# Kernel tuning notes

Measured on AMD Instinct MI355X. Metric: run time of the kernel, lower is better.

Reference implementation:

```python
import jax, jax.numpy as jnp
import numpy as np

N = 2_000_000  # number of Gaussians


def setup_inputs() -> dict:
    key = jax.random.key(0)
    k1, k2, k3 = jax.random.split(key, 3)
    quaternions = jax.random.normal(k1, (N, 4), dtype=jnp.float32)
    scales = jax.random.normal(k2, (N, 3), dtype=jnp.float32) * 0.5
    opacities = jax.random.normal(k3, (N, 1), dtype=jnp.float32)
    return {"quaternions": quaternions, "scales": scales, "opacities": opacities}


def quaternion_to_rotation_matrix(q):
    # q: [N,4] with layout (w, x, y, z) as in the torch source
    w, x, y, z = q[:, 0], q[:, 1], q[:, 2], q[:, 3]
    xx, yy, zz = x * x, y * y, z * z
    xy, xz, yz = x * y, x * z, y * z
    xw, yw, zw = x * w, y * w, z * w
    r0 = jnp.stack([1 - 2 * (yy + zz), 2 * (xy - zw), 2 * (xz + yw)], axis=-1)
    r1 = jnp.stack([2 * (xy + zw), 1 - 2 * (xx + zz), 2 * (yz - xw)], axis=-1)
    r2 = jnp.stack([2 * (xz - yw), 2 * (yz + xw), 1 - 2 * (xx + yy)], axis=-1)
    return jnp.stack([r0, r1, r2], axis=-2)  # [N,3,3]


def reference(quaternions, scales, opacities):
    # sigmoid applied to raw opacities (source: 1/(1+exp(-o)))
    opac = jax.nn.sigmoid(opacities)
    # NOTE: source normalizes by the GLOBAL Frobenius norm of the whole tensor
    # (to.linalg.norm with no dim) -- replicated faithfully.
    qn = quaternions / jnp.linalg.norm(quaternions)
    R = quaternion_to_rotation_matrix(qn)  # [N,3,3]
    # scales_d = (diag(exp(s)))**2 ; scales_i_d = (diag(1/exp(s)))**2
    s2 = jnp.exp(2.0 * scales)      # [N,3] diagonal of S^2
    inv_s2 = jnp.exp(-2.0 * scales)  # [N,3] diagonal of S^-2
    # cov = R @ diag(s2) @ R^T, inv_cov = R @ diag(inv_s2) @ R^T (closed form,
    # no batched 3x3 matmul chain / LAPACK inverse needed)
    cov = jnp.einsum('nij,nj,nkj->nik', R, s2, R)
    inv_cov = jnp.einsum('nij,nj,nkj->nik', R, inv_s2, R)
    return cov, inv_cov, opac
```

## Files before the change

kernel.cpp:

```cpp
#include <hip/hip_runtime.h>
#include <math.h>

#define RBLOCKS 1024
#define RTHREADS 256

__global__ __launch_bounds__(RTHREADS) void gp_reduce_sq(
    const float4* __restrict__ q4, int n4, double* __restrict__ partials) {
    __shared__ double sdata[RTHREADS];
    double acc = 0.0;
    int stride = gridDim.x * blockDim.x;
    for (int i = blockIdx.x * blockDim.x + threadIdx.x; i < n4; i += stride) {
        float4 v = q4[i];
        acc += (double)v.x * v.x + (double)v.y * v.y +
               (double)v.z * v.z + (double)v.w * v.w;
    }
    sdata[threadIdx.x] = acc;
    __syncthreads();
    for (int s = RTHREADS / 2; s > 0; s >>= 1) {
        if (threadIdx.x < s) sdata[threadIdx.x] += sdata[threadIdx.x + s];
        __syncthreads();
    }
    if (threadIdx.x == 0) partials[blockIdx.x] = sdata[0];
}

__global__ __launch_bounds__(RTHREADS) void gp_finalize_norm(
    const double* __restrict__ partials, float* __restrict__ inv_norm) {
    __shared__ double sdata[RTHREADS];
    double acc = 0.0;
    for (int i = threadIdx.x; i < RBLOCKS; i += RTHREADS) acc += partials[i];
    sdata[threadIdx.x] = acc;
    __syncthreads();
    for (int s = RTHREADS / 2; s > 0; s >>= 1) {
        if (threadIdx.x < s) sdata[threadIdx.x] += sdata[threadIdx.x + s];
        __syncthreads();
    }
    if (threadIdx.x == 0) *inv_norm = (float)(1.0 / sqrt(sdata[0]));
}

__global__ __launch_bounds__(256) void gp_main(
    const float4* __restrict__ q,
    const float* __restrict__ scales,
    const float* __restrict__ opac_in,
    const float* __restrict__ inv_norm_p,
    float* __restrict__ cov,
    float* __restrict__ inv_cov,
    float* __restrict__ opac_out,
    int n) {
    const float inv_norm = *inv_norm_p;
    int stride = gridDim.x * blockDim.x;
    for (int i = blockIdx.x * blockDim.x + threadIdx.x; i < n; i += stride) {
        float4 qi = q[i];
        float w = qi.x * inv_norm;
        float x = qi.y * inv_norm;
        float y = qi.z * inv_norm;
        float z = qi.w * inv_norm;

        float xx = x * x, yy = y * y, zz = z * z;
        float xy = x * y, xz = x * z, yz = y * z;
        float xw = x * w, yw = y * w, zw = z * w;

        float r00 = 1.f - 2.f * (yy + zz);
        float r01 = 2.f * (xy - zw);
        float r02 = 2.f * (xz + yw);
        float r10 = 2.f * (xy + zw);
        float r11 = 1.f - 2.f * (xx + zz);
        float r12 = 2.f * (yz - xw);
        float r20 = 2.f * (xz - yw);
        float r21 = 2.f * (yz + xw);
        float r22 = 1.f - 2.f * (xx + yy);

        float s0 = scales[3 * (size_t)i];
        float s1 = scales[3 * (size_t)i + 1];
        float s2 = scales[3 * (size_t)i + 2];

        float e0 = expf(2.f * s0), e1 = expf(2.f * s1), e2 = expf(2.f * s2);
        float f0 = expf(-2.f * s0), f1 = expf(-2.f * s1), f2 = expf(-2.f * s2);

        size_t base = (size_t)i * 9;

        {
            float a0 = r00 * e0, a1 = r01 * e1, a2 = r02 * e2;
            float b0 = r10 * e0, b1 = r11 * e1, b2 = r12 * e2;
            float c0 = r20 * e0, c1 = r21 * e1, c2 = r22 * e2;
            float m00 = a0 * r00 + a1 * r01 + a2 * r02;
            float m01 = a0 * r10 + a1 * r11 + a2 * r12;
            float m02 = a0 * r20 + a1 * r21 + a2 * r22;
            float m11 = b0 * r10 + b1 * r11 + b2 * r12;
            float m12 = b0 * r20 + b1 * r21 + b2 * r22;
            float m22 = c0 * r20 + c1 * r21 + c2 * r22;
            cov[base + 0] = m00;
            cov[base + 1] = m01;
            cov[base + 2] = m02;
            cov[base + 3] = m01;
            cov[base + 4] = m11;
            cov[base + 5] = m12;
            cov[base + 6] = m02;
            cov[base + 7] = m12;
            cov[base + 8] = m22;
        }
        {
            float a0 = r00 * f0, a1 = r01 * f1, a2 = r02 * f2;
            float b0 = r10 * f0, b1 = r11 * f1, b2 = r12 * f2;
            float c0 = r20 * f0, c1 = r21 * f1, c2 = r22 * f2;
            float m00 = a0 * r00 + a1 * r01 + a2 * r02;
            float m01 = a0 * r10 + a1 * r11 + a2 * r12;
            float m02 = a0 * r20 + a1 * r21 + a2 * r22;
            float m11 = b0 * r10 + b1 * r11 + b2 * r12;
            float m12 = b0 * r20 + b1 * r21 + b2 * r22;
            float m22 = c0 * r20 + c1 * r21 + c2 * r22;
            inv_cov[base + 0] = m00;
            inv_cov[base + 1] = m01;
            inv_cov[base + 2] = m02;
            inv_cov[base + 3] = m01;
            inv_cov[base + 4] = m11;
            inv_cov[base + 5] = m12;
            inv_cov[base + 6] = m02;
            inv_cov[base + 7] = m12;
            inv_cov[base + 8] = m22;
        }
        {
            float o = opac_in[i];
            opac_out[i] = 1.f / (1.f + expf(-o));
        }
    }
}

extern "C" void kernel_launch(void* const* d_in, const int* in_sizes, int n_in,
                              void* d_out, int out_size, void* d_ws, size_t ws_size,
                              hipStream_t stream) {
    const float* q = (const float*)d_in[0];
    const float* scales = (const float*)d_in[1];
    const float* opac = (const float*)d_in[2];
    int n = in_sizes[0] / 4;
    int n4 = in_sizes[0] / 4;

    float* out = (float*)d_out;
    float* cov = out;
    float* inv_cov = out + (size_t)n * 9;
    float* opac_out = out + (size_t)n * 18;

    double* partials = (double*)d_ws;
    float* inv_norm = (float*)((char*)d_ws + RBLOCKS * sizeof(double));

    gp_reduce_sq<<<RBLOCKS, RTHREADS, 0, stream>>>(
        (const float4*)q, n4, partials);
    gp_finalize_norm<<<1, RTHREADS, 0, stream>>>(partials, inv_norm);

    int blocks = 2048;
    gp_main<<<blocks, 256, 0, stream>>>(
        (const float4*)q, scales, opac, inv_norm,
        cov, inv_cov, opac_out, n);
}
```

Before: 51.31 us.

## Stage outputs through LDS for coalesced stores and fold norm finalize into main

The main kernel now processes one 256-element chunk per block. Scales are loaded as float4 into shared memory, and both 3x3 outputs are staged in LDS and written back as coalesced float4 stores, replacing stride-9 scalar stores. The separate finalize-norm launch is removed: every block re-reduces the 1024 double partials itself to get the inverse norm. The inverse exponentials are computed as reciprocals of the forward exps. In exchange, the kernel uses more LDS and has redundant per-block reduction work, and the grid grows to about 7800 blocks.

```diff
diff --git a/kernel.cpp b/kernel.cpp
--- a/kernel.cpp
+++ b/kernel.cpp
@@ -3,6 +3,7 @@
 
 #define RBLOCKS 1024
 #define RTHREADS 256
+#define CHUNK 256
 
 __global__ __launch_bounds__(RTHREADS) void gp_reduce_sq(
     const float4* __restrict__ q4, int n4, double* __restrict__ partials) {
@@ -23,33 +24,61 @@
     if (threadIdx.x == 0) partials[blockIdx.x] = sdata[0];
 }
 
-__global__ __launch_bounds__(RTHREADS) void gp_finalize_norm(
-    const double* __restrict__ partials, float* __restrict__ inv_norm) {
-    __shared__ double sdata[RTHREADS];
-    double acc = 0.0;
-    for (int i = threadIdx.x; i < RBLOCKS; i += RTHREADS) acc += partials[i];
-    sdata[threadIdx.x] = acc;
-    __syncthreads();
-    for (int s = RTHREADS / 2; s > 0; s >>= 1) {
-        if (threadIdx.x < s) sdata[threadIdx.x] += sdata[threadIdx.x + s];
-        __syncthreads();
-    }
-    if (threadIdx.x == 0) *inv_norm = (float)(1.0 / sqrt(sdata[0]));
-}
-
 __global__ __launch_bounds__(256) void gp_main(
     const float4* __restrict__ q,
     const float* __restrict__ scales,
     const float* __restrict__ opac_in,
-    const float* __restrict__ inv_norm_p,
+    const double* __restrict__ partials,
     float* __restrict__ cov,
     float* __restrict__ inv_cov,
     float* __restrict__ opac_out,
     int n) {
-    const float inv_norm = *inv_norm_p;
-    int stride = gridDim.x * blockDim.x;
-    for (int i = blockIdx.x * blockDim.x + threadIdx.x; i < n; i += stride) {
-        float4 qi = q[i];
+    __shared__ union SU {
+        double red[4];
+        float mat[2 * CHUNK * 9];
+    } u;
+    __shared__ float s_sc[CHUNK * 3];
+
+    const int tid = threadIdx.x;
+    const int c0 = blockIdx.x * CHUNK;
+    const int count = min(CHUNK, n - c0);
+
+    float4 qi = make_float4(0.f, 0.f, 0.f, 0.f);
+    float op = 0.f;
+    if (tid < count) {
+        qi = q[c0 + tid];
+        op = opac_in[c0 + tid];
+    }
+    const int nsf = count * 3;
+    const int nsf4 = nsf >> 2;
+    const float4* sc4 = (const float4*)(scales + (size_t)c0 * 3);
+    float4 sv = make_float4(0.f, 0.f, 0.f, 0.f);
+    if (tid < nsf4) sv = sc4[tid];
+
+    double acc = 0.0;
+#pragma unroll
+    for (int k = 0; k < RBLOCKS / 256; ++k) acc += partials[tid + 256 * k];
+#pragma unroll
+    for (int off = 32; off > 0; off >>= 1) acc += __shfl_down(acc, off);
+    if ((tid & 63) == 0) u.red[tid >> 6] = acc;
+
+    if (tid < nsf4) {
+        s_sc[4 * tid + 0] = sv.x;
+        s_sc[4 * tid + 1] = sv.y;
+        s_sc[4 * tid + 2] = sv.z;
+        s_sc[4 * tid + 3] = sv.w;
+    }
+    {
+        int r = nsf - nsf4 * 4;
+        if (tid < r) s_sc[nsf4 * 4 + tid] = scales[(size_t)c0 * 3 + nsf4 * 4 + tid];
+    }
+    __syncthreads();
+
+    double tot = u.red[0] + u.red[1] + u.red[2] + u.red[3];
+    const float inv_norm = (float)(1.0 / sqrt(tot));
+    __syncthreads();
+
+    if (tid < count) {
         float w = qi.x * inv_norm;
         float x = qi.y * inv_norm;
         float y = qi.z * inv_norm;
@@ -69,59 +98,58 @@
         float r21 = 2.f * (yz + xw);
         float r22 = 1.f - 2.f * (xx + yy);
 
-        float s0 = scales[3 * (size_t)i];
-        float s1 = scales[3 * (size_t)i + 1];
-        float s2 = scales[3 * (size_t)i + 2];
+        float s0 = s_sc[3 * tid + 0];
+        float s1 = s_sc[3 * tid + 1];
+        float s2 = s_sc[3 * tid + 2];
 
         float e0 = expf(2.f * s0), e1 = expf(2.f * s1), e2 = expf(2.f * s2);
-        float f0 = expf(-2.f * s0), f1 = expf(-2.f * s1), f2 = expf(-2.f * s2);
+        float f0 = 1.f / e0, f1 = 1.f / e1, f2 = 1.f / e2;
 
-        size_t base = (size_t)i * 9;
-
+        float* mc = &u.mat[tid * 9];
+        float* mi = &u.mat[CHUNK * 9 + tid * 9];
         {
             float a0 = r00 * e0, a1 = r01 * e1, a2 = r02 * e2;
             float b0 = r10 * e0, b1 = r11 * e1, b2 = r12 * e2;
-            float c0 = r20 * e0, c1 = r21 * e1, c2 = r22 * e2;
+            float c0_ = r20 * e0, c1 = r21 * e1, c2 = r22 * e2;
             float m00 = a0 * r00 + a1 * r01 + a2 * r02;
             float m01 = a0 * r10 + a1 * r11 + a2 * r12;
             float m02 = a0 * r20 + a1 * r21 + a2 * r22;
             float m11 = b0 * r10 + b1 * r11 + b2 * r12;
             float m12 = b0 * r20 + b1 * r21 + b2 * r22;
-            float m22 = c0 * r20 + c1 * r21 + c2 * r22;
-            cov[base + 0] = m00;
-            cov[base + 1] = m01;
-            cov[base + 2] = m02;
-            cov[base + 3] = m01;
-            cov[base + 4] = m11;
-            cov[base + 5] = m12;
-            cov[base + 6] = m02;
-            cov[base + 7] = m12;
-            cov[base + 8] = m22;
+            float m22 = c0_ * r20 + c1 * r21 + c2 * r22;
+            mc[0] = m00; mc[1] = m01; mc[2] = m02;
+            mc[3] = m01; mc[4] = m11; mc[5] = m12;
+            mc[6] = m02; mc[7] = m12; mc[8] = m22;
         }
         {
             float a0 = r00 * f0, a1 = r01 * f1, a2 = r02 * f2;
             float b0 = r10 * f0, b1 = r11 * f1, b2 = r12 * f2;
-            float c0 = r20 * f0, c1 = r21 * f1, c2 = r22 * f2;
+            float c0_ = r20 * f0, c1 = r21 * f1, c2 = r22 * f2;
             float m00 = a0 * r00 + a1 * r01 + a2 * r02;
             float m01 = a0 * r10 + a1 * r11 + a2 * r12;
             float m02 = a0 * r20 + a1 * r21 + a2 * r22;
             float m11 = b0 * r10 + b1 * r11 + b2 * r12;
             float m12 = b0 * r20 + b1 * r21 + b2 * r22;
-            float m22 = c0 * r20 + c1 * r21 + c2 * r22;
-            inv_cov[base + 0] = m00;
-            inv_cov[base + 1] = m01;
-            inv_cov[base + 2] = m02;
-            inv_cov[base + 3] = m01;
-            inv_cov[base + 4] = m11;
-            inv_cov[base + 5] = m12;
-            inv_cov[base + 6] = m02;
-            inv_cov[base + 7] = m12;
-            inv_cov[base + 8] = m22;
+            float m22 = c0_ * r20 + c1 * r21 + c2 * r22;
+            mi[0] = m00; mi[1] = m01; mi[2] = m02;
+            mi[3] = m01; mi[4] = m11; mi[5] = m12;
+            mi[6] = m02; mi[7] = m12; mi[8] = m22;
         }
-        {
-            float o = opac_in[i];
-            opac_out[i] = 1.f / (1.f + expf(-o));
-        }
+        opac_out[c0 + tid] = 1.f / (1.f + expf(-op));
+    }
+    __syncthreads();
+
+    const int nf = count * 9;
+    const int nfv = nf >> 2;
+    float4* covo = (float4*)(cov + (size_t)c0 * 9);
+    float4* invo = (float4*)(inv_cov + (size_t)c0 * 9);
+    const float4* mc4 = (const float4*)u.mat;
+    const float4* mi4 = (const float4*)(u.mat + CHUNK * 9);
+    for (int j = tid; j < nfv; j += 256) covo[j] = mc4[j];
+    for (int j = tid; j < nfv; j += 256) invo[j] = mi4[j];
+    for (int j = nfv * 4 + tid; j < nf; j += 256) {
+        cov[(size_t)c0 * 9 + j] = u.mat[j];
+        inv_cov[(size_t)c0 * 9 + j] = u.mat[CHUNK * 9 + j];
     }
 }
 
@@ -132,7 +160,6 @@
     const float* scales = (const float*)d_in[1];
     const float* opac = (const float*)d_in[2];
     int n = in_sizes[0] / 4;
-    int n4 = in_sizes[0] / 4;
 
     float* out = (float*)d_out;
     float* cov = out;
@@ -140,14 +167,11 @@
     float* opac_out = out + (size_t)n * 18;
 
     double* partials = (double*)d_ws;
-    float* inv_norm = (float*)((char*)d_ws + RBLOCKS * sizeof(double));
 
-    gp_reduce_sq<<<RBLOCKS, RTHREADS, 0, stream>>>(
-        (const float4*)q, n4, partials);
-    gp_finalize_norm<<<1, RTHREADS, 0, stream>>>(partials, inv_norm);
+    gp_reduce_sq<<<RBLOCKS, RTHREADS, 0, stream>>>((const float4*)q, n, partials);
 
-    int blocks = 2048;
-    gp_main<<<blocks, 256, 0, stream>>>(
-        (const float4*)q, scales, opac, inv_norm,
+    int nblocks = (n + CHUNK - 1) / CHUNK;
+    gp_main<<<nblocks, 256, 0, stream>>>(
+        (const float4*)q, scales, opac, partials,
         cov, inv_cov, opac_out, n);
 }
```

Measured after the change: 44.72 us. 12.8% less time.
